# Kernel tuning notes

Measured on AMD Instinct MI355X. Metric: run time of the kernel, lower is better.

## Reference

```python
import jax, jax.numpy as jnp
import numpy as np
import math

S, B, D, H = 1024, 4, 1024, 16
DH = D // H


def setup_inputs() -> dict:
    key = jax.random.key(0)
    ks = jax.random.split(key, 8)
    hidden_states = jax.random.normal(ks[0], (S, B, D), dtype=jnp.float32)
    u = jax.random.uniform(ks[1], (B, 1, 1, S), dtype=jnp.float32)
    attention_mask = jnp.where(u < 0.2, jnp.float32(-10000.0), jnp.float32(0.0))
    std = 0.02
    Wq = jax.random.normal(ks[2], (D, D), dtype=jnp.float32) * std
    bq = jnp.zeros((D,), dtype=jnp.float32)
    Wk = jax.random.normal(ks[3], (D, D), dtype=jnp.float32) * std
    bk = jnp.zeros((D,), dtype=jnp.float32)
    Wv = jax.random.normal(ks[4], (D, D), dtype=jnp.float32) * std
    bv = jnp.zeros((D,), dtype=jnp.float32)
    return {"hidden_states": hidden_states, "attention_mask": attention_mask,
            "Wq": Wq, "bq": bq, "Wk": Wk, "bk": bk, "Wv": Wv, "bv": bv}


def _split_heads(x):
    # [S,B,D] -> [B,H,S,DH]
    s, b, d = x.shape
    return x.reshape(s, b, H, DH).transpose(1, 2, 0, 3)


def reference(hidden_states, attention_mask, Wq, bq, Wk, bk, Wv, bv):
    scale = 1.0 / math.sqrt(DH)
    q = _split_heads(hidden_states @ Wq.T + bq)  # [B,H,S,DH]
    k = _split_heads(hidden_states @ Wk.T + bk)
    v = _split_heads(hidden_states @ Wv.T + bv)
    # scaled scores + additive mask (mask [B,1,1,S] broadcasts over heads, query pos)
    scores = jnp.einsum('bhsd,bhtd->bhst', q, k) * scale + attention_mask  # [B,H,S,S]
    probs = jax.nn.softmax(scores, axis=-1)
    # NOTE: original forward's dropout block is a no-op (only reshapes), so none applied
    ctx = jnp.einsum('bhst,bhtd->bhsd', probs, v)  # [B,H,S,DH]
    # -> [S,B,D]
    return ctx.transpose(2, 0, 1, 3).reshape(S, B, D)
```

## Files before the change

### kernel.cpp

```cpp
#include <hip/hip_runtime.h>
#include <hip/hip_bf16.h>

#define S_LEN  1024
#define BATCH  4
#define DMODEL 1024
#define NHEAD  16
#define DHEAD  64
#define NROWS  (S_LEN*BATCH)

typedef __bf16 bf16;
typedef __bf16 bf16x4 __attribute__((ext_vector_type(4)));
typedef __bf16 bf16x8 __attribute__((ext_vector_type(8)));
typedef float  f32x4  __attribute__((ext_vector_type(4)));

#define AS1 __attribute__((address_space(1)))
#define AS3 __attribute__((address_space(3)))

#define LOG2E   1.4426950408889634f
#define QSCALE  0.18033688011112042f

__device__ __forceinline__ void gload16(const bf16* g, bf16* l) {
  __builtin_amdgcn_global_load_lds((const AS1 void*)g, (AS3 void*)l, 16, 0, 0);
}

__device__ __forceinline__ float fast_exp2(float x) {
#if __has_builtin(__builtin_amdgcn_exp2f)
  return __builtin_amdgcn_exp2f(x);
#else
  return exp2f(x);
#endif
}

__global__ __launch_bounds__(256) void cvt_all(
    const float* __restrict__ hs, const float* __restrict__ wq,
    const float* __restrict__ wk, const float* __restrict__ wv,
    bf16* __restrict__ Xb, bf16* __restrict__ Wb)
{
  const int b = blockIdx.x;
  const float* src; bf16* dst; int i;
  if (b < 2048)      { src = hs; dst = Xb;                           i = b*256        + threadIdx.x; }
  else if (b < 2560) { src = wq; dst = Wb;                           i = (b-2048)*256 + threadIdx.x; }
  else if (b < 3072) { src = wk; dst = Wb + (size_t)DMODEL*DMODEL;   i = (b-2560)*256 + threadIdx.x; }
  else               { src = wv; dst = Wb + (size_t)2*DMODEL*DMODEL; i = (b-3072)*256 + threadIdx.x; }
  const float4* s4 = (const float4*)src;
  float4 a = s4[2*i], c = s4[2*i+1];
  bf16x8 o;
  o[0]=(bf16)a.x; o[1]=(bf16)a.y; o[2]=(bf16)a.z; o[3]=(bf16)a.w;
  o[4]=(bf16)c.x; o[5]=(bf16)c.y; o[6]=(bf16)c.z; o[7]=(bf16)c.w;
  ((bf16x8*)dst)[i] = o;
}

#define BM 128
#define BN 128
#define BK 32

__global__ __launch_bounds__(256) void qkv_gemm(
    const bf16* __restrict__ X, const bf16* __restrict__ Wcat,
    const float* __restrict__ bq, const float* __restrict__ bk, const float* __restrict__ bv,
    bf16* __restrict__ Qo, bf16* __restrict__ Ko, bf16* __restrict__ Vo)
{
  __shared__ __align__(16) bf16 As[BM*BK];
  __shared__ __align__(16) bf16 Bs[BN*BK];

  const int tid  = threadIdx.x;
  const int row0 = blockIdx.x * BM;
  const int col0 = blockIdx.y * BN;
  const int wsel = col0 >> 10;
  const int coln = col0 & 1023;

  const int wv   = tid >> 6;
  const int lane = tid & 63;
  const int lg   = lane >> 4;
  const int lr   = lane & 15;
  const int wr   = (wv >> 1) << 6;
  const int wc   = (wv & 1) << 6;

  const int c0 = tid, c1 = tid + 256;
  const size_t gA0 = (size_t)(row0 + (c0>>2))*DMODEL + (size_t)((c0&3)<<3);
  const size_t gA1 = (size_t)(row0 + (c1>>2))*DMODEL + (size_t)((c1&3)<<3);
  const size_t gB0 = (size_t)(col0 + (c0>>2))*DMODEL + (size_t)((c0&3)<<3);
  const size_t gB1 = (size_t)(col0 + (c1>>2))*DMODEL + (size_t)((c1&3)<<3);
  const int wb = (tid >> 6) << 6;
  bf16* lA0 = As + (size_t)wb*8;
  bf16* lA1 = As + (size_t)(wb+256)*8;
  bf16* lB0 = Bs + (size_t)wb*8;
  bf16* lB1 = Bs + (size_t)(wb+256)*8;

  f32x4 acc[4][4];
  #pragma unroll
  for (int mi=0; mi<4; ++mi)
    #pragma unroll
    for (int ni=0; ni<4; ++ni)
      acc[mi][ni] = (f32x4){0.f,0.f,0.f,0.f};

  for (int k0 = 0; k0 < DMODEL; k0 += BK) {
    __syncthreads();
    gload16(X    + gA0 + k0, lA0);
    gload16(X    + gA1 + k0, lA1);
    gload16(Wcat + gB0 + k0, lB0);
    gload16(Wcat + gB1 + k0, lB1);
    __syncthreads();

    bf16x8 af[4], bfr[4];
    #pragma unroll
    for (int mi=0; mi<4; ++mi)
      af[mi] = *(const bf16x8*)&As[(wr + mi*16 + lr)*BK + lg*8];
    #pragma unroll
    for (int ni=0; ni<4; ++ni)
      bfr[ni] = *(const bf16x8*)&Bs[(wc + ni*16 + lr)*BK + lg*8];

    #pragma unroll
    for (int mi=0; mi<4; ++mi)
      #pragma unroll
      for (int ni=0; ni<4; ++ni)
        acc[mi][ni] = __builtin_amdgcn_mfma_f32_16x16x32_bf16(af[mi], bfr[ni], acc[mi][ni], 0, 0, 0);
  }

  const float* bias = (wsel==0) ? bq : ((wsel==1) ? bk : bv);
  bf16* Out = (wsel==0) ? Qo : ((wsel==1) ? Ko : Vo);
  const float oscale = (wsel==0) ? QSCALE : 1.0f;

  #pragma unroll
  for (int ni=0; ni<4; ++ni) {
    const int co = coln + wc + ni*16 + lr;
    const float bias_v = bias[co];
    const int h  = co >> 6;
    const int dh = co & 63;
    #pragma unroll
    for (int mi=0; mi<4; ++mi) {
      #pragma unroll
      for (int p=0; p<4; ++p) {
        const int gr = row0 + wr + mi*16 + lg*4 + p;
        const int s_ = gr >> 2;
        const int b_ = gr & 3;
        Out[((size_t)(b_*NHEAD + h)*S_LEN + s_)*DHEAD + dh] = (bf16)((acc[mi][ni][p] + bias_v) * oscale);
      }
    }
  }
}

#define LPAD 72

__global__ __launch_bounds__(256, 4) void attn_mfma(
    const bf16* __restrict__ Q, const bf16* __restrict__ K, const bf16* __restrict__ V,
    const float* __restrict__ mask, float* __restrict__ out)
{
  __shared__ __align__(16) bf16 Ks[64*LPAD];
  __shared__ __align__(16) bf16 Vt[64*LPAD];
  __shared__ __align__(16) bf16 Pw[4][16][LPAD];
  __shared__ bf16 Msk[S_LEN];

  const int bh   = blockIdx.x;
  const int b_   = bh >> 4;
  const int h    = bh & 15;
  const int tid  = threadIdx.x;
  const int wv   = tid >> 6;
  const int lane = tid & 63;
  const int lg   = lane >> 4;
  const int lr   = lane & 15;
  const int q0   = blockIdx.y * 64;

  {
    const float4 m4 = *(const float4*)&mask[(size_t)b_*S_LEN + tid*4];
    bf16x4 mm;
    mm[0]=(bf16)(m4.x*LOG2E); mm[1]=(bf16)(m4.y*LOG2E);
    mm[2]=(bf16)(m4.z*LOG2E); mm[3]=(bf16)(m4.w*LOG2E);
    *(bf16x4*)&Msk[tid*4] = mm;
  }

  const bf16* Qb = Q + ((size_t)bh*S_LEN + q0 + wv*16 + lr)*DHEAD;
  const bf16x8 qa0 = *(const bf16x8*)&Qb[lg*8];
  const bf16x8 qa1 = *(const bf16x8*)&Qb[32 + lg*8];

  const bf16* Kb = K + (size_t)bh*S_LEN*DHEAD;
  const bf16* Vb = V + (size_t)bh*S_LEN*DHEAD;

  const int kr = tid >> 2, kc = (tid & 3) << 4;
  const int vr = tid & 63, vc = (tid >> 6) << 4;

  bf16x8 kreg0 = *(const bf16x8*)&Kb[(size_t)kr*DHEAD + kc];
  bf16x8 kreg1 = *(const bf16x8*)&Kb[(size_t)kr*DHEAD + kc + 8];
  bf16x8 vreg0 = *(const bf16x8*)&Vb[(size_t)vr*DHEAD + vc];
  bf16x8 vreg1 = *(const bf16x8*)&Vb[(size_t)vr*DHEAD + vc + 8];
  *(bf16x8*)&Ks[kr*LPAD + kc]     = kreg0;
  *(bf16x8*)&Ks[kr*LPAD + kc + 8] = kreg1;
  #pragma unroll
  for (int i=0;i<8;++i){ Vt[(vc+i)*LPAD + vr] = vreg0[i]; Vt[(vc+8+i)*LPAD + vr] = vreg1[i]; }
  __syncthreads();

  f32x4 ctx[4];
  #pragma unroll
  for (int nt=0; nt<4; ++nt) ctx[nt] = (f32x4){0.f,0.f,0.f,0.f};
  float lsum[4] = {0.f,0.f,0.f,0.f};

  for (int t = 0; t < 16; ++t) {
    if (t < 15) {
      const size_t nb = (size_t)(t+1)*64;
      kreg0 = *(const bf16x8*)&Kb[(nb+kr)*DHEAD + kc];
      kreg1 = *(const bf16x8*)&Kb[(nb+kr)*DHEAD + kc + 8];
      vreg0 = *(const bf16x8*)&Vb[(nb+vr)*DHEAD + vc];
      vreg1 = *(const bf16x8*)&Vb[(nb+vr)*DHEAD + vc + 8];
    }

    f32x4 sacc[4];
    __builtin_amdgcn_s_setprio(1);
    #pragma unroll
    for (int nt=0; nt<4; ++nt) {
      sacc[nt] = (f32x4){0.f,0.f,0.f,0.f};
      bf16x8 kb0 = *(const bf16x8*)&Ks[(nt*16 + lr)*LPAD + lg*8];
      bf16x8 kb1 = *(const bf16x8*)&Ks[(nt*16 + lr)*LPAD + 32 + lg*8];
      sacc[nt] = __builtin_amdgcn_mfma_f32_16x16x32_bf16(qa0, kb0, sacc[nt], 0,0,0);
      sacc[nt] = __builtin_amdgcn_mfma_f32_16x16x32_bf16(qa1, kb1, sacc[nt], 0,0,0);
    }
    __builtin_amdgcn_s_setprio(0);

    const int tb = t*64;
    #pragma unroll
    for (int nt=0; nt<4; ++nt) {
      const float mval = (float)Msk[tb + nt*16 + lr];
      #pragma unroll
      for (int p=0; p<4; ++p) {
        const float pr = fast_exp2(sacc[nt][p] + mval);
        lsum[p] += pr;
        Pw[wv][lg*4 + p][nt*16 + lr] = (bf16)pr;
      }
    }

    {
      bf16x8 pa0 = *(const bf16x8*)&Pw[wv][lr][lg*8];
      bf16x8 pa1 = *(const bf16x8*)&Pw[wv][lr][32 + lg*8];
      __builtin_amdgcn_s_setprio(1);
      #pragma unroll
      for (int nt=0; nt<4; ++nt) {
        bf16x8 vb0 = *(const bf16x8*)&Vt[(nt*16 + lr)*LPAD + lg*8];
        bf16x8 vb1 = *(const bf16x8*)&Vt[(nt*16 + lr)*LPAD + 32 + lg*8];
        ctx[nt] = __builtin_amdgcn_mfma_f32_16x16x32_bf16(pa0, vb0, ctx[nt], 0,0,0);
        ctx[nt] = __builtin_amdgcn_mfma_f32_16x16x32_bf16(pa1, vb1, ctx[nt], 0,0,0);
      }
      __builtin_amdgcn_s_setprio(0);
    }

    __syncthreads();
    if (t < 15) {
      *(bf16x8*)&Ks[kr*LPAD + kc]     = kreg0;
      *(bf16x8*)&Ks[kr*LPAD + kc + 8] = kreg1;
      #pragma unroll
      for (int i=0;i<8;++i){ Vt[(vc+i)*LPAD + vr] = vreg0[i]; Vt[(vc+8+i)*LPAD + vr] = vreg1[i]; }
      __syncthreads();
    }
  }

  #pragma unroll
  for (int p=0; p<4; ++p) {
    float s = lsum[p];
    s += __shfl_xor(s, 1); s += __shfl_xor(s, 2);
    s += __shfl_xor(s, 4); s += __shfl_xor(s, 8);
    lsum[p] = s;
  }

  #pragma unroll
  for (int p=0; p<4; ++p) {
    const float inv = 1.f / lsum[p];
    const int qg = q0 + wv*16 + lg*4 + p;
    float* op = out + ((size_t)qg*BATCH + b_)*DMODEL + h*DHEAD;
    #pragma unroll
    for (int nt=0; nt<4; ++nt) op[nt*16 + lr] = ctx[nt][p] * inv;
  }
}

extern "C" void kernel_launch(void* const* d_in, const int* in_sizes, int n_in,
                              void* d_out, int out_size, void* d_ws, size_t ws_size,
                              hipStream_t stream) {
  const float* hs   = (const float*)d_in[0];
  const float* mask = (const float*)d_in[1];
  const float* Wq   = (const float*)d_in[2];
  const float* bq   = (const float*)d_in[3];
  const float* Wk   = (const float*)d_in[4];
  const float* bk   = (const float*)d_in[5];
  const float* Wv   = (const float*)d_in[6];
  const float* bv   = (const float*)d_in[7];
  float* out = (float*)d_out;

  char* ws = (char*)d_ws;
  bf16* Xb = (bf16*)ws;
  bf16* Wb = Xb + (size_t)NROWS*DMODEL;
  bf16* Qw = Wb + (size_t)3*DMODEL*DMODEL;
  bf16* Kw = Qw + (size_t)NROWS*DMODEL;
  bf16* Vw = Kw + (size_t)NROWS*DMODEL;

  cvt_all<<<3584, 256, 0, stream>>>(hs, Wq, Wk, Wv, Xb, Wb);

  qkv_gemm<<<dim3(NROWS/BM, 3*DMODEL/BN), 256, 0, stream>>>(Xb, Wb, bq, bk, bv, Qw, Kw, Vw);

  attn_mfma<<<dim3(BATCH*NHEAD, S_LEN/64), 256, 0, stream>>>(Qw, Kw, Vw, mask, out);
}
```

Before: 83.37 us.

## Double-buffer K/V tiles and process 128 queries per 512-thread attention block

The attention kernel now uses 8 waves per block covering 128 query rows, so each K/V tile loaded into shared memory is reused by twice as many queries and global K/V traffic is halved. K and V tiles are double-buffered in LDS, which removes one of the two block barriers per iteration by writing the next tile into the other buffer. The trade-off is more LDS per block, half as many blocks in the grid, and a 512-thread launch bound that may lower occupancy.

After: 78.57 us. 5.8% less time.

```diff
diff --git a/kernel.cpp b/kernel.cpp
--- a/kernel.cpp
+++ b/kernel.cpp
@@ -140,14 +140,15 @@
 }
 
 #define LPAD 72
-
-__global__ __launch_bounds__(256, 4) void attn_mfma(
+#define QBLK 128
+
+__global__ __launch_bounds__(512, 4) void attn_mfma(
     const bf16* __restrict__ Q, const bf16* __restrict__ K, const bf16* __restrict__ V,
     const float* __restrict__ mask, float* __restrict__ out)
 {
-  __shared__ __align__(16) bf16 Ks[64*LPAD];
-  __shared__ __align__(16) bf16 Vt[64*LPAD];
-  __shared__ __align__(16) bf16 Pw[4][16][LPAD];
+  __shared__ __align__(16) bf16 KsBuf[2][64*LPAD];
+  __shared__ __align__(16) bf16 VtBuf[2][64*LPAD];
+  __shared__ __align__(16) bf16 Pw[8][16][LPAD];
   __shared__ bf16 Msk[S_LEN];
 
   const int bh   = blockIdx.x;
@@ -158,9 +159,9 @@
   const int lane = tid & 63;
   const int lg   = lane >> 4;
   const int lr   = lane & 15;
-  const int q0   = blockIdx.y * 64;
-
-  {
+  const int q0   = blockIdx.y * QBLK;
+
+  if (tid < 256) {
     const float4 m4 = *(const float4*)&mask[(size_t)b_*S_LEN + tid*4];
     bf16x4 mm;
     mm[0]=(bf16)(m4.x*LOG2E); mm[1]=(bf16)(m4.y*LOG2E);
@@ -175,17 +176,14 @@
   const bf16* Kb = K + (size_t)bh*S_LEN*DHEAD;
   const bf16* Vb = V + (size_t)bh*S_LEN*DHEAD;
 
-  const int kr = tid >> 2, kc = (tid & 3) << 4;
-  const int vr = tid & 63, vc = (tid >> 6) << 4;
-
-  bf16x8 kreg0 = *(const bf16x8*)&Kb[(size_t)kr*DHEAD + kc];
-  bf16x8 kreg1 = *(const bf16x8*)&Kb[(size_t)kr*DHEAD + kc + 8];
-  bf16x8 vreg0 = *(const bf16x8*)&Vb[(size_t)vr*DHEAD + vc];
-  bf16x8 vreg1 = *(const bf16x8*)&Vb[(size_t)vr*DHEAD + vc + 8];
-  *(bf16x8*)&Ks[kr*LPAD + kc]     = kreg0;
-  *(bf16x8*)&Ks[kr*LPAD + kc + 8] = kreg1;
-  #pragma unroll
-  for (int i=0;i<8;++i){ Vt[(vc+i)*LPAD + vr] = vreg0[i]; Vt[(vc+8+i)*LPAD + vr] = vreg1[i]; }
+  const int kr = tid >> 3, kc = (tid & 7) << 3;
+  const int vr = tid & 63, vc = (tid >> 6) << 3;
+
+  bf16x8 kreg = *(const bf16x8*)&Kb[(size_t)kr*DHEAD + kc];
+  bf16x8 vreg = *(const bf16x8*)&Vb[(size_t)vr*DHEAD + vc];
+  *(bf16x8*)&KsBuf[0][kr*LPAD + kc] = kreg;
+  #pragma unroll
+  for (int i=0;i<8;++i) VtBuf[0][(vc+i)*LPAD + vr] = vreg[i];
   __syncthreads();
 
   f32x4 ctx[4];
@@ -194,12 +192,13 @@
   float lsum[4] = {0.f,0.f,0.f,0.f};
 
   for (int t = 0; t < 16; ++t) {
+    const bf16* Kc = KsBuf[t & 1];
+    const bf16* Vc = VtBuf[t & 1];
+
     if (t < 15) {
       const size_t nb = (size_t)(t+1)*64;
-      kreg0 = *(const bf16x8*)&Kb[(nb+kr)*DHEAD + kc];
-      kreg1 = *(const bf16x8*)&Kb[(nb+kr)*DHEAD + kc + 8];
-      vreg0 = *(const bf16x8*)&Vb[(nb+vr)*DHEAD + vc];
-      vreg1 = *(const bf16x8*)&Vb[(nb+vr)*DHEAD + vc + 8];
+      kreg = *(const bf16x8*)&Kb[(nb+kr)*DHEAD + kc];
+      vreg = *(const bf16x8*)&Vb[(nb+vr)*DHEAD + vc];
     }
 
     f32x4 sacc[4];
@@ -207,8 +206,8 @@
     #pragma unroll
     for (int nt=0; nt<4; ++nt) {
       sacc[nt] = (f32x4){0.f,0.f,0.f,0.f};
-      bf16x8 kb0 = *(const bf16x8*)&Ks[(nt*16 + lr)*LPAD + lg*8];
-      bf16x8 kb1 = *(const bf16x8*)&Ks[(nt*16 + lr)*LPAD + 32 + lg*8];
+      bf16x8 kb0 = *(const bf16x8*)&Kc[(nt*16 + lr)*LPAD + lg*8];
+      bf16x8 kb1 = *(const bf16x8*)&Kc[(nt*16 + lr)*LPAD + 32 + lg*8];
       sacc[nt] = __builtin_amdgcn_mfma_f32_16x16x32_bf16(qa0, kb0, sacc[nt], 0,0,0);
       sacc[nt] = __builtin_amdgcn_mfma_f32_16x16x32_bf16(qa1, kb1, sacc[nt], 0,0,0);
     }
@@ -232,22 +231,22 @@
       __builtin_amdgcn_s_setprio(1);
       #pragma unroll
       for (int nt=0; nt<4; ++nt) {
-        bf16x8 vb0 = *(const bf16x8*)&Vt[(nt*16 + lr)*LPAD + lg*8];
-        bf16x8 vb1 = *(const bf16x8*)&Vt[(nt*16 + lr)*LPAD + 32 + lg*8];
+        bf16x8 vb0 = *(const bf16x8*)&Vc[(nt*16 + lr)*LPAD + lg*8];
+        bf16x8 vb1 = *(const bf16x8*)&Vc[(nt*16 + lr)*LPAD + 32 + lg*8];
         ctx[nt] = __builtin_amdgcn_mfma_f32_16x16x32_bf16(pa0, vb0, ctx[nt], 0,0,0);
         ctx[nt] = __builtin_amdgcn_mfma_f32_16x16x32_bf16(pa1, vb1, ctx[nt], 0,0,0);
       }
       __builtin_amdgcn_s_setprio(0);
     }
 
+    if (t < 15) {
+      bf16* Kn = (bf16*)KsBuf[(t+1) & 1];
+      bf16* Vn = (bf16*)VtBuf[(t+1) & 1];
+      *(bf16x8*)&Kn[kr*LPAD + kc] = kreg;
+      #pragma unroll
+      for (int i=0;i<8;++i) Vn[(vc+i)*LPAD + vr] = vreg[i];
+    }
     __syncthreads();
-    if (t < 15) {
-      *(bf16x8*)&Ks[kr*LPAD + kc]     = kreg0;
-      *(bf16x8*)&Ks[kr*LPAD + kc + 8] = kreg1;
-      #pragma unroll
-      for (int i=0;i<8;++i){ Vt[(vc+i)*LPAD + vr] = vreg0[i]; Vt[(vc+8+i)*LPAD + vr] = vreg1[i]; }
-      __syncthreads();
-    }
   }
 
   #pragma unroll
@@ -292,5 +291,5 @@
 
   qkv_gemm<<<dim3(NROWS/BM, 3*DMODEL/BN), 256, 0, stream>>>(Xb, Wb, bq, bk, bv, Qw, Kw, Vw);
 
-  attn_mfma<<<dim3(BATCH*NHEAD, S_LEN/64), 256, 0, stream>>>(Qw, Kw, Vw, mask, out);
-}
+  attn_mfma<<<dim3(BATCH*NHEAD, S_LEN/QBLK), 512, 0, stream>>>(Qw, Kw, Vw, mask, out);
+}
```
